# Kernel optimization log

Measured on AMD Instinct MI355X. Metric: run time of the kernel, lower is better.

## Reference

```python
import jax, jax.numpy as jnp
import numpy as np


def setup_inputs() -> dict:
    key = jax.random.key(0)
    ks = jax.random.split(key, 8)
    B, C, W, H = 4, 256, 64, 64
    Ck = C // 8  # 32, key/query channels
    x = jax.random.normal(ks[0], (B, C, W, H), dtype=jnp.float32)
    # 1x1 conv weights (xavier-uniform-like scale), biases zero per init_conv
    sf = (6.0 / (C + Ck)) ** 0.5
    sh = (6.0 / (C + C)) ** 0.5
    Wf = jax.random.uniform(ks[1], (Ck, C), jnp.float32, -sf, sf)
    Wg = jax.random.uniform(ks[2], (Ck, C), jnp.float32, -sf, sf)
    Wh = jax.random.uniform(ks[3], (C, C), jnp.float32, -sh, sh)
    bf = jnp.zeros((Ck,), jnp.float32)
    bg = jnp.zeros((Ck,), jnp.float32)
    bh = jnp.zeros((C,), jnp.float32)
    gamma = jax.random.uniform(ks[4], (1,), jnp.float32) * 0.5
    return {"x": x, "Wf": Wf, "bf": bf, "Wg": Wg, "bg": bg,
            "Wh": Wh, "bh": bh, "gamma": gamma}


def reference(x, Wf, bf, Wg, bg, Wh, bh, gamma):
    B, C, W, H = x.shape
    N = W * H
    xf = x.reshape(B, C, N)  # [B, C, N]
    # 1x1 convs == per-pixel linear maps
    f = jnp.einsum('kc,bcn->bkn', Wf, xf) + bf[None, :, None]  # [B, C/8, N]
    g = jnp.einsum('kc,bcn->bkn', Wg, xf) + bg[None, :, None]  # [B, C/8, N]
    h = jnp.einsum('oc,bcn->bon', Wh, xf) + bh[None, :, None]  # [B, C,   N]
    # attention[b, i, j] = sum_k f[b,k,i] * g[b,k,j]; softmax over j
    attn = jax.nn.softmax(jnp.einsum('bki,bkj->bij', f, g), axis=-1)  # [B,N,N]
    # bmm(h, attention): out[b,c,i] = sum_j h[b,c,j] * attn[b,j,i]
    sa = jnp.einsum('bcj,bji->bci', h, attn).reshape(B, C, W, H)
    return gamma[0] * sa + x
```

## Files before the change

### kernel.cpp

```cpp
#include <hip/hip_runtime.h>

#define NB 4
#define NC 256
#define NCK 32
#define NPIX 4096

typedef unsigned short u16;
typedef unsigned int u32;
typedef __bf16 bfv8 __attribute__((ext_vector_type(8)));
typedef float f32x4 __attribute__((ext_vector_type(4)));
#define LOG2E 1.4426950408889634f

__device__ inline u16 f2bf(float f) {
  union { float f; u32 u; } v; v.f = f;
  u32 r = v.u + 0x7fffu + ((v.u >> 16) & 1u);
  return (u16)(r >> 16);
}
__device__ inline float bf2f(u16 h) {
  union { u32 u; float f; } v; v.u = (u32)h << 16; return v.f;
}
__device__ inline u32 cvtpk(float a, float b) {
  u32 r;
  asm("v_cvt_pk_bf16_f32 %0, %1, %2" : "=v"(r) : "v"(a), "v"(b));
  return r;
}

__global__ __launch_bounds__(256) void k_fg(const float* __restrict__ x,
                                            const float* __restrict__ Wf,
                                            const float* __restrict__ bf_,
                                            const float* __restrict__ Wg,
                                            const float* __restrict__ bg_,
                                            u16* __restrict__ fP,
                                            u16* __restrict__ gT,
                                            u16* __restrict__ xT) {
  __shared__ float Wt[256][65];
  __shared__ float xl[32][68];
  __shared__ float tb[64][68];
  int blk = blockIdx.x;
  int b = blk >> 6;
  int n0 = (blk & 63) * 64;
  int t = threadIdx.x;
  int tx = t & 15, ty = t >> 4;
  for (int r = 0; r < 64; r++) {
    float w = (r < 32) ? Wf[r * 256 + t] : Wg[(r - 32) * 256 + t];
    Wt[t][r] = w;
  }
  float acc[4][4] = {};
  int n = t >> 2, cp = t & 3;
  for (int kc = 0; kc < 8; kc++) {
    __syncthreads();
#pragma unroll
    for (int r = 0; r < 2; r++) {
      int e = (r * 256 + t) * 4;
      int row = e >> 6, col = e & 63;
      *(float4*)&xl[row][col] =
          *(const float4*)(x + ((size_t)(b * NC + kc * 32 + row)) * NPIX + n0 + col);
    }
    __syncthreads();
    {
      u32 uu[4];
#pragma unroll
      for (int q = 0; q < 4; q++)
        uu[q] = cvtpk(xl[cp * 8 + 2 * q][n], xl[cp * 8 + 2 * q + 1][n]);
      *(uint4*)(xT + ((size_t)(b * NPIX) + n0 + n) * NC + kc * 32 + cp * 8) =
          make_uint4(uu[0], uu[1], uu[2], uu[3]);
    }
#pragma unroll
    for (int kk = 0; kk < 32; kk++) {
      float4 xv = *(const float4*)&xl[kk][tx * 4];
      float w0 = Wt[kc * 32 + kk][ty * 4 + 0];
      float w1 = Wt[kc * 32 + kk][ty * 4 + 1];
      float w2 = Wt[kc * 32 + kk][ty * 4 + 2];
      float w3 = Wt[kc * 32 + kk][ty * 4 + 3];
      acc[0][0] += w0 * xv.x; acc[0][1] += w0 * xv.y; acc[0][2] += w0 * xv.z; acc[0][3] += w0 * xv.w;
      acc[1][0] += w1 * xv.x; acc[1][1] += w1 * xv.y; acc[1][2] += w1 * xv.z; acc[1][3] += w1 * xv.w;
      acc[2][0] += w2 * xv.x; acc[2][1] += w2 * xv.y; acc[2][2] += w2 * xv.z; acc[2][3] += w2 * xv.w;
      acc[3][0] += w3 * xv.x; acc[3][1] += w3 * xv.y; acc[3][2] += w3 * xv.z; acc[3][3] += w3 * xv.w;
    }
  }
#pragma unroll
  for (int j = 0; j < 4; j++) {
    int o = ty * 4 + j;
    float bias = (o < 32) ? bf_[o] : bg_[o - 32];
#pragma unroll
    for (int vi = 0; vi < 4; vi++) tb[tx * 4 + vi][o] = acc[j][vi] + bias;
  }
  __syncthreads();
  int part = t & 3;
  {
    u32 ph[4], plo[4];
#pragma unroll
    for (int e = 0; e < 4; e++) {
      float v0 = tb[n][part * 8 + 2 * e + 0];
      float v1 = tb[n][part * 8 + 2 * e + 1];
      u16 h0 = f2bf(v0), h1 = f2bf(v1);
      u16 l0 = f2bf(v0 - bf2f(h0)), l1 = f2bf(v1 - bf2f(h1));
      ph[e] = (u32)h0 | ((u32)h1 << 16);
      plo[e] = (u32)l0 | ((u32)l1 << 16);
    }
    int jt_g = (n0 >> 4) + (n >> 4), r = n & 15;
    u16* dst = fP + ((size_t)(b * 256) + jt_g) * 1024 + r * 32 + part * 8;
    *(uint4*)dst = make_uint4(ph[0], ph[1], ph[2], ph[3]);
    *(uint4*)(dst + 512) = make_uint4(plo[0], plo[1], plo[2], plo[3]);
  }
  {
    u32 ph[4], plo[4];
#pragma unroll
    for (int e = 0; e < 4; e++) {
      float v0 = tb[n][32 + part * 8 + 2 * e + 0];
      float v1 = tb[n][32 + part * 8 + 2 * e + 1];
      u16 h0 = f2bf(v0), h1 = f2bf(v1);
      u16 l0 = f2bf(v0 - bf2f(h0)), l1 = f2bf(v1 - bf2f(h1));
      ph[e] = (u32)h0 | ((u32)h1 << 16);
      plo[e] = (u32)l0 | ((u32)l1 << 16);
    }
    u16* dst = gT + ((size_t)(b * NPIX) + n0 + n) * 64 + part * 8;
    *(uint4*)dst = make_uint4(ph[0], ph[1], ph[2], ph[3]);
    *(uint4*)(dst + 32) = make_uint4(plo[0], plo[1], plo[2], plo[3]);
  }
}

__global__ __launch_bounds__(256) void k_h(const u16* __restrict__ xT,
                                           const float* __restrict__ Wh,
                                           const float* __restrict__ bh,
                                           u16* __restrict__ h2) {
  __shared__ u16 At[128 * 32];
  __shared__ u16 Bt[128 * 32];
  int blk = blockIdx.x;
  int b = blk >> 6, r = blk & 63;
  int nt = r >> 1, ot = r & 1;
  int n0 = nt * 128, o0 = ot * 128;
  int t = threadIdx.x, lane = t & 63, w = t >> 6;
  int wr = w >> 1, wc = w & 1;
  int coll = lane & 15, cg = lane >> 4;
  f32x4 acc[4][4] = {};
  for (int kc = 0; kc < 8; kc++) {
    __syncthreads();
#pragma unroll
    for (int r2 = 0; r2 < 2; r2++) {
      int s = r2 * 256 + t;
      int row = s >> 2, slot = s & 3;
      int sw = (row ^ (row >> 2)) & 3;
      uint4 va = *(const uint4*)(xT + ((size_t)(b * NPIX + n0 + row)) * NC + kc * 32 + slot * 8);
      *(uint4*)((char*)At + row * 64 + ((slot ^ sw) * 16)) = va;
      const float* wsrc = Wh + (size_t)(o0 + row) * NC + kc * 32 + slot * 8;
      float4 w0 = *(const float4*)wsrc;
      float4 w1 = *(const float4*)(wsrc + 4);
      uint4 vb = make_uint4(cvtpk(w0.x, w0.y), cvtpk(w0.z, w0.w),
                            cvtpk(w1.x, w1.y), cvtpk(w1.z, w1.w));
      *(uint4*)((char*)Bt + row * 64 + ((slot ^ sw) * 16)) = vb;
    }
    __syncthreads();
    bfv8 af[4], bfr[4];
#pragma unroll
    for (int mi = 0; mi < 4; mi++) {
      int row = wr * 64 + mi * 16 + coll;
      int slot = cg ^ ((row ^ (row >> 2)) & 3);
      af[mi] = *(const bfv8*)((const char*)At + row * 64 + slot * 16);
    }
#pragma unroll
    for (int ni = 0; ni < 4; ni++) {
      int row = wc * 64 + ni * 16 + coll;
      int slot = cg ^ ((row ^ (row >> 2)) & 3);
      bfr[ni] = *(const bfv8*)((const char*)Bt + row * 64 + slot * 16);
    }
#pragma unroll
    for (int mi = 0; mi < 4; mi++)
#pragma unroll
      for (int ni = 0; ni < 4; ni++)
        acc[mi][ni] = __builtin_amdgcn_mfma_f32_16x16x32_bf16(af[mi], bfr[ni], acc[mi][ni], 0, 0, 0);
  }
#pragma unroll
  for (int ni = 0; ni < 4; ni++) {
    int o = o0 + wc * 64 + ni * 16 + coll;
    float bias = bh[o];
#pragma unroll
    for (int mi = 0; mi < 4; mi++) {
      int px = n0 + wr * 64 + mi * 16 + cg * 4;
      u32 lo = cvtpk(acc[mi][ni][0] + bias, acc[mi][ni][1] + bias);
      u32 hi = cvtpk(acc[mi][ni][2] + bias, acc[mi][ni][3] + bias);
      *(uint2*)(h2 + (((size_t)(b * 128) + (px >> 5)) * NC + o) * 32 + (px & 31)) =
          make_uint2(lo, hi);
    }
  }
}

__global__ __launch_bounds__(256) void k_pass1(const u16* __restrict__ fP,
                                               const u16* __restrict__ gT,
                                               float2* __restrict__ pmd) {
  __shared__ u16 gs[64 * 64];
  int blk = blockIdx.x;
  int iq = blk & 7, jt = (blk >> 3) & 63, b = blk >> 9;
  int j0 = jt * 64, ibase = iq * 512;
  int t = threadIdx.x, lane = t & 63, w = t >> 6;
  int coll = lane & 15, cg = lane >> 4;
  const u16* fr = fP + ((size_t)(b * 256) + (j0 >> 4) + w) * 1024 + coll * 32 + cg * 8;
  bfv8 ah = *(const bfv8*)fr;
  bfv8 al = *(const bfv8*)(fr + 512);
  float m[4] = {-3e38f, -3e38f, -3e38f, -3e38f}, d[4] = {0.f, 0.f, 0.f, 0.f};
  int r0 = t >> 3, s0 = t & 7;
  uint4 v0 = *(const uint4*)(gT + ((size_t)(b * NPIX) + ibase + r0) * 64 + s0 * 8);
  uint4 v1 = *(const uint4*)(gT + ((size_t)(b * NPIX) + ibase + 32 + r0) * 64 + s0 * 8);
  for (int it2 = 0; it2 < 8; ++it2) {
    __syncthreads();
    *(uint4*)(&gs[r0 * 64 + ((s0 ^ (r0 & 7)) << 3)]) = v0;
    *(uint4*)(&gs[(32 + r0) * 64 + ((s0 ^ (r0 & 7)) << 3)]) = v1;
    __syncthreads();
    if (it2 < 7) {
      v0 = *(const uint4*)(gT + ((size_t)(b * NPIX) + ibase + (it2 + 1) * 64 + r0) * 64 + s0 * 8);
      v1 = *(const uint4*)(gT + ((size_t)(b * NPIX) + ibase + (it2 + 1) * 64 + 32 + r0) * 64 + s0 * 8);
    }
    float sv[4][4];
#pragma unroll
    for (int t4 = 0; t4 < 4; ++t4) {
      int row = t4 * 16 + coll;
      const u16* base = &gs[row * 64];
      bfv8 bh = *(const bfv8*)(base + ((cg ^ (row & 7)) << 3));
      bfv8 bl = *(const bfv8*)(base + (((4 + cg) ^ (row & 7)) << 3));
      f32x4 s = {0.f, 0.f, 0.f, 0.f};
      s = __builtin_amdgcn_mfma_f32_16x16x32_bf16(al, bh, s, 0, 0, 0);
      s = __builtin_amdgcn_mfma_f32_16x16x32_bf16(ah, bl, s, 0, 0, 0);
      s = __builtin_amdgcn_mfma_f32_16x16x32_bf16(ah, bh, s, 0, 0, 0);
      sv[t4][0] = s[0]; sv[t4][1] = s[1]; sv[t4][2] = s[2]; sv[t4][3] = s[3];
    }
#pragma unroll
    for (int r = 0; r < 4; ++r) {
      float ms = fmaxf(fmaxf(sv[0][r], sv[1][r]), fmaxf(sv[2][r], sv[3][r]));
      float nm = fmaxf(m[r], ms);
      d[r] = d[r] * __expf(m[r] - nm) + __expf(sv[0][r] - nm) + __expf(sv[1][r] - nm) +
             __expf(sv[2][r] - nm) + __expf(sv[3][r] - nm);
      m[r] = nm;
    }
  }
#pragma unroll
  for (int r = 0; r < 4; ++r) {
#pragma unroll
    for (int off = 1; off < 16; off <<= 1) {
      float m2 = __shfl_xor(m[r], off);
      float d2 = __shfl_xor(d[r], off);
      float nm = fmaxf(m[r], m2);
      d[r] = d[r] * __expf(m[r] - nm) + d2 * __expf(m2 - nm);
      m[r] = nm;
    }
  }
  if (coll == 0) {
#pragma unroll
    for (int r = 0; r < 4; ++r) {
      int j = j0 + w * 16 + cg * 4 + r;
      pmd[((size_t)(b * 8 + iq)) * NPIX + j] = make_float2(m[r], d[r]);
    }
  }
}

__global__ __launch_bounds__(256) void k_comb(const float2* __restrict__ pmd,
                                              float* __restrict__ aout) {
  int idx = blockIdx.x * 256 + threadIdx.x;
  int b = idx >> 12, j = idx & 4095;
  float2 p[8];
  float M = -3e38f;
#pragma unroll
  for (int q = 0; q < 8; ++q) {
    p[q] = pmd[((size_t)(b * 8 + q)) * NPIX + j];
    M = fmaxf(M, p[q].x);
  }
  float D = 0.f;
#pragma unroll
  for (int q = 0; q < 8; ++q) D += p[q].y * __expf(p[q].x - M);
  aout[idx] = fmaf(M, LOG2E, __log2f(D));
}

__global__ __launch_bounds__(512, 2) void k_pass2(const u16* __restrict__ fP,
                                                  const u16* __restrict__ gT,
                                                  const u16* __restrict__ h2,
                                                  const float* __restrict__ arow,
                                                  const float* __restrict__ x,
                                                  const float* __restrict__ gamma,
                                                  float* __restrict__ out) {
  __shared__ char smem[18944];
  int blk = blockIdx.x;
  int it = blk & 63, b = blk >> 6;
  int i0 = it * 64;
  int t = threadIdx.x, lane = t & 63, w = t >> 6;
  int coll = lane & 15, cg = lane >> 4;
  int jt_w = w & 3, ihalf = w >> 2;
  int cbase = w * 32;
  int swz = (coll & 7) << 4;
  float* alds = (float*)(smem + 16384);
  bfv8 gah[2], gal[2];
#pragma unroll
  for (int q = 0; q < 2; ++q) {
    const u16* gr = gT + ((size_t)(b * NPIX) + i0 + (ihalf * 2 + q) * 16 + coll) * 64 + cg * 8;
    gah[q] = *(const bfv8*)gr;
    gal[q] = *(const bfv8*)(gr + 32);
  }
  f32x4 acc[2][4] = {};
  const u16* h2b = h2 + ((size_t)(b * 128) * NC + cbase + coll) * 32 + cg * 8;
  bfv8 hv[2][2];
#pragma unroll
  for (int ct = 0; ct < 2; ++ct)
#pragma unroll
    for (int kb = 0; kb < 2; ++kb)
      hv[ct][kb] = *(const bfv8*)(h2b + (size_t)kb * 8192 + ct * 512);
  const u16* fPb = fP + ((size_t)(b * 256)) * 1024 + coll * 32 + cg * 8;
  bfv8 fh = *(const bfv8*)(fPb + jt_w * 1024);
  bfv8 fl = *(const bfv8*)(fPb + jt_w * 1024 + 512);
  float apre = 0.f;
  if (t < 64) alds[t] = arow[b * NPIX + t];
  f32x4 s[2];
#pragma unroll
  for (int q = 0; q < 2; ++q) {
    f32x4 ss = {0.f, 0.f, 0.f, 0.f};
    ss = __builtin_amdgcn_mfma_f32_16x16x32_bf16(fl, gah[q], ss, 0, 0, 0);
    ss = __builtin_amdgcn_mfma_f32_16x16x32_bf16(fh, gal[q], ss, 0, 0, 0);
    ss = __builtin_amdgcn_mfma_f32_16x16x32_bf16(fh, gah[q], ss, 0, 0, 0);
    s[q] = ss;
  }
  fh = *(const bfv8*)(fPb + (4 + jt_w) * 1024);
  fl = *(const bfv8*)(fPb + (4 + jt_w) * 1024 + 512);
  if (t < 64) apre = arow[b * NPIX + 64 + t];
  __syncthreads();

  for (int jc = 0; jc < 64; ++jc) {
    int p = jc & 1;
    {
      int jr = jt_w * 16 + cg * 4;
      float4 av = *(const float4*)&alds[p * 64 + jr];
#pragma unroll
      for (int q = 0; q < 2; ++q) {
        float p0 = exp2f(fmaf(s[q][0], LOG2E, -av.x));
        float p1 = exp2f(fmaf(s[q][1], LOG2E, -av.y));
        float p2 = exp2f(fmaf(s[q][2], LOG2E, -av.z));
        float p3 = exp2f(fmaf(s[q][3], LOG2E, -av.w));
        char* pb = smem + p * 8192 + (ihalf * 2 + q) * 2048 + coll * 128;
        *(uint2*)(pb + ((jt_w * 32 + cg * 8) ^ swz)) =
            make_uint2(cvtpk(p0, p1), cvtpk(p2, p3));
      }
    }
    if (t < 64) alds[((jc + 1) & 1) * 64 + t] = apre;
    __syncthreads();
#pragma unroll
    for (int ni = 0; ni < 4; ++ni) {
      const char* pbr = smem + p * 8192 + ni * 2048 + coll * 128;
      bfv8 pa0 = *(const bfv8*)(pbr + ((cg * 16) ^ swz));
      bfv8 pa1 = *(const bfv8*)(pbr + ((64 + cg * 16) ^ swz));
#pragma unroll
      for (int ct = 0; ct < 2; ++ct) {
        acc[ct][ni] = __builtin_amdgcn_mfma_f32_16x16x32_bf16(hv[ct][0], pa0, acc[ct][ni], 0, 0, 0);
        acc[ct][ni] = __builtin_amdgcn_mfma_f32_16x16x32_bf16(hv[ct][1], pa1, acc[ct][ni], 0, 0, 0);
      }
    }
    if (jc < 63) {
#pragma unroll
      for (int ct = 0; ct < 2; ++ct)
#pragma unroll
        for (int kb = 0; kb < 2; ++kb)
          hv[ct][kb] = *(const bfv8*)(h2b + (size_t)((jc + 1) * 2 + kb) * 8192 + ct * 512);
#pragma unroll
      for (int q = 0; q < 2; ++q) {
        f32x4 ss = {0.f, 0.f, 0.f, 0.f};
        ss = __builtin_amdgcn_mfma_f32_16x16x32_bf16(fl, gah[q], ss, 0, 0, 0);
        ss = __builtin_amdgcn_mfma_f32_16x16x32_bf16(fh, gal[q], ss, 0, 0, 0);
        ss = __builtin_amdgcn_mfma_f32_16x16x32_bf16(fh, gah[q], ss, 0, 0, 0);
        s[q] = ss;
      }
      if (jc < 62) {
        fh = *(const bfv8*)(fPb + (size_t)((jc + 2) * 4 + jt_w) * 1024);
        fl = *(const bfv8*)(fPb + (size_t)((jc + 2) * 4 + jt_w) * 1024 + 512);
        if (t < 64) apre = arow[b * NPIX + (jc + 2) * 64 + t];
      }
    }
  }
  float gam = gamma[0];
  int row = lane >> 2, part = lane & 3;
#pragma unroll
  for (int rd = 0; rd < 4; ++rd) {
    int ct = rd >> 1, ih = rd & 1;
    __syncthreads();
    float* tbf = (float*)(smem + w * 2304);
#pragma unroll
    for (int nq = 0; nq < 2; ++nq)
#pragma unroll
      for (int r = 0; r < 4; ++r)
        tbf[(cg * 4 + r) * 36 + nq * 16 + coll] = acc[ct][ih * 2 + nq][r];
    __syncthreads();
    const float* src = tbf + row * 36 + part * 8;
    size_t off = ((size_t)(b * NC) + cbase + ct * 16 + row) * NPIX + i0 + ih * 32 + part * 8;
    float4 x0 = *(const float4*)(x + off);
    float4 x1 = *(const float4*)(x + off + 4);
    float4 o0, o1;
    o0.x = fmaf(gam, src[0], x0.x); o0.y = fmaf(gam, src[1], x0.y);
    o0.z = fmaf(gam, src[2], x0.z); o0.w = fmaf(gam, src[3], x0.w);
    o1.x = fmaf(gam, src[4], x1.x); o1.y = fmaf(gam, src[5], x1.y);
    o1.z = fmaf(gam, src[6], x1.z); o1.w = fmaf(gam, src[7], x1.w);
    *(float4*)(out + off) = o0;
    *(float4*)(out + off + 4) = o1;
  }
}

extern "C" void kernel_launch(void* const* d_in, const int* in_sizes, int n_in,
                              void* d_out, int out_size, void* d_ws, size_t ws_size,
                              hipStream_t stream) {
  (void)in_sizes; (void)n_in; (void)out_size; (void)ws_size;
  const float* x = (const float*)d_in[0];
  const float* Wf = (const float*)d_in[1];
  const float* bf_ = (const float*)d_in[2];
  const float* Wg = (const float*)d_in[3];
  const float* bg_ = (const float*)d_in[4];
  const float* Wh = (const float*)d_in[5];
  const float* bh = (const float*)d_in[6];
  const float* gamma = (const float*)d_in[7];
  float* out = (float*)d_out;
  char* ws = (char*)d_ws;
  const size_t M1 = 1u << 20;
  u16* xT = (u16*)ws;
  u16* h2 = (u16*)(ws + 9 * M1);
  u16* fP = (u16*)(ws + 17 * M1);
  u16* gT = (u16*)(ws + 19 * M1);
  float* aout = (float*)(ws + 21 * M1);
  float2* pmd = (float2*)(ws + 21 * M1 + (1u << 17));

  k_fg<<<256, 256, 0, stream>>>(x, Wf, bf_, Wg, bg_, fP, gT, xT);
  k_pass1<<<2048, 256, 0, stream>>>(fP, gT, pmd);
  k_h<<<256, 256, 0, stream>>>(xT, Wh, bh, h2);
  k_comb<<<64, 256, 0, stream>>>(pmd, aout);
  k_pass2<<<256, 512, 0, stream>>>(fP, gT, h2, aout, x, gamma, out);
}
```

Before: 117.9 us.

## Double the j-chunk per iteration in pass2 to halve barrier count

Widens the attention-key chunk handled per loop iteration from 64 to 128 columns, so each wave computes two sets of score tiles, writes twice as many probabilities into a larger shared-memory P buffer, and runs four K-steps of MFMA per accumulator instead of two. This halves the number of loop iterations and __syncthreads barriers and lengthens each MFMA burst. In exchange, shared memory grows from about 19KB to 34KB per block and the f, h and s register footprint roughly doubles, which could lower occupancy under launch_bounds(512,2) or cause spills.

```diff
diff --git a/kernel.cpp b/kernel.cpp
--- a/kernel.cpp
+++ b/kernel.cpp
@@ -276,7 +276,7 @@
                                                   const float* __restrict__ x,
                                                   const float* __restrict__ gamma,
                                                   float* __restrict__ out) {
-  __shared__ char smem[18944];
+  __shared__ char smem[33792];
   int blk = blockIdx.x;
   int it = blk & 63, b = blk >> 6;
   int i0 = it * 64;
@@ -285,7 +285,7 @@
   int jt_w = w & 3, ihalf = w >> 2;
   int cbase = w * 32;
   int swz = (coll & 7) << 4;
-  float* alds = (float*)(smem + 16384);
+  float* alds = (float*)(smem + 32768);
   bfv8 gah[2], gal[2];
 #pragma unroll
   for (int q = 0; q < 2; ++q) {
@@ -295,78 +295,95 @@
   }
   f32x4 acc[2][4] = {};
   const u16* h2b = h2 + ((size_t)(b * 128) * NC + cbase + coll) * 32 + cg * 8;
-  bfv8 hv[2][2];
+  bfv8 hv[2][4];
 #pragma unroll
   for (int ct = 0; ct < 2; ++ct)
 #pragma unroll
-    for (int kb = 0; kb < 2; ++kb)
+    for (int kb = 0; kb < 4; ++kb)
       hv[ct][kb] = *(const bfv8*)(h2b + (size_t)kb * 8192 + ct * 512);
   const u16* fPb = fP + ((size_t)(b * 256)) * 1024 + coll * 32 + cg * 8;
-  bfv8 fh = *(const bfv8*)(fPb + jt_w * 1024);
-  bfv8 fl = *(const bfv8*)(fPb + jt_w * 1024 + 512);
+  bfv8 fh[2], fl[2];
+#pragma unroll
+  for (int cq = 0; cq < 2; ++cq) {
+    fh[cq] = *(const bfv8*)(fPb + (cq * 4 + jt_w) * 1024);
+    fl[cq] = *(const bfv8*)(fPb + (cq * 4 + jt_w) * 1024 + 512);
+  }
   float apre = 0.f;
-  if (t < 64) alds[t] = arow[b * NPIX + t];
-  f32x4 s[2];
-#pragma unroll
-  for (int q = 0; q < 2; ++q) {
-    f32x4 ss = {0.f, 0.f, 0.f, 0.f};
-    ss = __builtin_amdgcn_mfma_f32_16x16x32_bf16(fl, gah[q], ss, 0, 0, 0);
-    ss = __builtin_amdgcn_mfma_f32_16x16x32_bf16(fh, gal[q], ss, 0, 0, 0);
-    ss = __builtin_amdgcn_mfma_f32_16x16x32_bf16(fh, gah[q], ss, 0, 0, 0);
-    s[q] = ss;
-  }
-  fh = *(const bfv8*)(fPb + (4 + jt_w) * 1024);
-  fl = *(const bfv8*)(fPb + (4 + jt_w) * 1024 + 512);
-  if (t < 64) apre = arow[b * NPIX + 64 + t];
+  if (t < 128) alds[t] = arow[b * NPIX + t];
+  f32x4 s[2][2];
+#pragma unroll
+  for (int cq = 0; cq < 2; ++cq)
+#pragma unroll
+    for (int q = 0; q < 2; ++q) {
+      f32x4 ss = {0.f, 0.f, 0.f, 0.f};
+      ss = __builtin_amdgcn_mfma_f32_16x16x32_bf16(fl[cq], gah[q], ss, 0, 0, 0);
+      ss = __builtin_amdgcn_mfma_f32_16x16x32_bf16(fh[cq], gal[q], ss, 0, 0, 0);
+      ss = __builtin_amdgcn_mfma_f32_16x16x32_bf16(fh[cq], gah[q], ss, 0, 0, 0);
+      s[cq][q] = ss;
+    }
+#pragma unroll
+  for (int cq = 0; cq < 2; ++cq) {
+    fh[cq] = *(const bfv8*)(fPb + (8 + cq * 4 + jt_w) * 1024);
+    fl[cq] = *(const bfv8*)(fPb + (8 + cq * 4 + jt_w) * 1024 + 512);
+  }
+  if (t < 128) apre = arow[b * NPIX + 128 + t];
   __syncthreads();
 
-  for (int jc = 0; jc < 64; ++jc) {
+  for (int jc = 0; jc < 32; ++jc) {
     int p = jc & 1;
     {
       int jr = jt_w * 16 + cg * 4;
-      float4 av = *(const float4*)&alds[p * 64 + jr];
-#pragma unroll
-      for (int q = 0; q < 2; ++q) {
-        float p0 = exp2f(fmaf(s[q][0], LOG2E, -av.x));
-        float p1 = exp2f(fmaf(s[q][1], LOG2E, -av.y));
-        float p2 = exp2f(fmaf(s[q][2], LOG2E, -av.z));
-        float p3 = exp2f(fmaf(s[q][3], LOG2E, -av.w));
-        char* pb = smem + p * 8192 + (ihalf * 2 + q) * 2048 + coll * 128;
-        *(uint2*)(pb + ((jt_w * 32 + cg * 8) ^ swz)) =
-            make_uint2(cvtpk(p0, p1), cvtpk(p2, p3));
+#pragma unroll
+      for (int cq = 0; cq < 2; ++cq) {
+        float4 av = *(const float4*)&alds[p * 128 + cq * 64 + jr];
+#pragma unroll
+        for (int q = 0; q < 2; ++q) {
+          float p0 = exp2f(fmaf(s[cq][q][0], LOG2E, -av.x));
+          float p1 = exp2f(fmaf(s[cq][q][1], LOG2E, -av.y));
+          float p2 = exp2f(fmaf(s[cq][q][2], LOG2E, -av.z));
+          float p3 = exp2f(fmaf(s[cq][q][3], LOG2E, -av.w));
+          char* pb = smem + p * 16384 + (ihalf * 2 + q) * 4096 + coll * 256;
+          *(uint2*)(pb + (((cq * 4 + jt_w) * 32 + cg * 8) ^ swz)) =
+              make_uint2(cvtpk(p0, p1), cvtpk(p2, p3));
+        }
       }
     }
-    if (t < 64) alds[((jc + 1) & 1) * 64 + t] = apre;
+    if (t < 128) alds[((jc + 1) & 1) * 128 + t] = apre;
     __syncthreads();
 #pragma unroll
     for (int ni = 0; ni < 4; ++ni) {
-      const char* pbr = smem + p * 8192 + ni * 2048 + coll * 128;
-      bfv8 pa0 = *(const bfv8*)(pbr + ((cg * 16) ^ swz));
-      bfv8 pa1 = *(const bfv8*)(pbr + ((64 + cg * 16) ^ swz));
-#pragma unroll
-      for (int ct = 0; ct < 2; ++ct) {
-        acc[ct][ni] = __builtin_amdgcn_mfma_f32_16x16x32_bf16(hv[ct][0], pa0, acc[ct][ni], 0, 0, 0);
-        acc[ct][ni] = __builtin_amdgcn_mfma_f32_16x16x32_bf16(hv[ct][1], pa1, acc[ct][ni], 0, 0, 0);
+      const char* pbr = smem + p * 16384 + ni * 4096 + coll * 256;
+#pragma unroll
+      for (int kb = 0; kb < 4; ++kb) {
+        bfv8 pa = *(const bfv8*)(pbr + ((kb * 64 + cg * 16) ^ swz));
+#pragma unroll
+        for (int ct = 0; ct < 2; ++ct)
+          acc[ct][ni] = __builtin_amdgcn_mfma_f32_16x16x32_bf16(hv[ct][kb], pa, acc[ct][ni], 0, 0, 0);
       }
     }
-    if (jc < 63) {
+    if (jc < 31) {
 #pragma unroll
       for (int ct = 0; ct < 2; ++ct)
 #pragma unroll
-        for (int kb = 0; kb < 2; ++kb)
-          hv[ct][kb] = *(const bfv8*)(h2b + (size_t)((jc + 1) * 2 + kb) * 8192 + ct * 512);
-#pragma unroll
-      for (int q = 0; q < 2; ++q) {
-        f32x4 ss = {0.f, 0.f, 0.f, 0.f};
-        ss = __builtin_amdgcn_mfma_f32_16x16x32_bf16(fl, gah[q], ss, 0, 0, 0);
-        ss = __builtin_amdgcn_mfma_f32_16x16x32_bf16(fh, gal[q], ss, 0, 0, 0);
-        ss = __builtin_amdgcn_mfma_f32_16x16x32_bf16(fh, gah[q], ss, 0, 0, 0);
-        s[q] = ss;
-      }
-      if (jc < 62) {
-        fh = *(const bfv8*)(fPb + (size_t)((jc + 2) * 4 + jt_w) * 1024);
-        fl = *(const bfv8*)(fPb + (size_t)((jc + 2) * 4 + jt_w) * 1024 + 512);
-        if (t < 64) apre = arow[b * NPIX + (jc + 2) * 64 + t];
+        for (int kb = 0; kb < 4; ++kb)
+          hv[ct][kb] = *(const bfv8*)(h2b + (size_t)((jc + 1) * 4 + kb) * 8192 + ct * 512);
+#pragma unroll
+      for (int cq = 0; cq < 2; ++cq)
+#pragma unroll
+        for (int q = 0; q < 2; ++q) {
+          f32x4 ss = {0.f, 0.f, 0.f, 0.f};
+          ss = __builtin_amdgcn_mfma_f32_16x16x32_bf16(fl[cq], gah[q], ss, 0, 0, 0);
+          ss = __builtin_amdgcn_mfma_f32_16x16x32_bf16(fh[cq], gal[q], ss, 0, 0, 0);
+          ss = __builtin_amdgcn_mfma_f32_16x16x32_bf16(fh[cq], gah[q], ss, 0, 0, 0);
+          s[cq][q] = ss;
+        }
+      if (jc < 30) {
+#pragma unroll
+        for (int cq = 0; cq < 2; ++cq) {
+          fh[cq] = *(const bfv8*)(fPb + (size_t)((jc + 2) * 8 + cq * 4 + jt_w) * 1024);
+          fl[cq] = *(const bfv8*)(fPb + (size_t)((jc + 2) * 8 + cq * 4 + jt_w) * 1024 + 512);
+        }
+        if (t < 128) apre = arow[b * NPIX + (jc + 2) * 128 + t];
       }
     }
   }
```

After: 124.1 us. 1.05x slower.
